# Performance work log

Measured on AMD Instinct MI355X. Metric: run time of the kernel, lower is better.

## Reference

```python
import jax, jax.numpy as jnp
import numpy as np

K = 2            # negative:positive edge ratio (init arg k)
N_NODES = 4096
N_EDGES = 8192
FEAT = 64


def setup_inputs() -> dict:
    key = jax.random.key(0)
    k1, k2, k3 = jax.random.split(key, 3)
    node_feature = jax.random.normal(k1, (N_NODES, FEAT), dtype=jnp.float32)
    edge_src = jax.random.randint(k2, (N_EDGES,), 0, N_NODES, dtype=jnp.int32)
    edge_dst = jax.random.randint(k3, (N_EDGES,), 0, N_NODES, dtype=jnp.int32)
    return {"node_feature": node_feature, "edge_src": edge_src, "edge_dst": edge_dst}


def reference(node_feature, edge_src, edge_dst):
    E = edge_src.shape[0]
    N = node_feature.shape[0]
    # [E, E] pairwise mask: candidate column j is valid for row i iff
    # dst[j] != dst[i] and dst[j] != src[i]
    valid = (edge_dst[:, None] != edge_dst[None, :]) & (edge_src[:, None] != edge_dst[None, :])
    # unsorted_segment_min over rows grouped by edge_src -> [N, E]
    segmin = jax.ops.segment_min(valid.astype(jnp.int8), edge_src, num_segments=N)
    # gather back per edge -> [E, E], flatten
    m = segmin[edge_src].reshape(-1).astype(bool)  # [E*E]
    num_negatives = jnp.sum(m)
    ratio = num_negatives // E                      # integer ratio as in TF code
    keep_prob = (K / ratio).astype(jnp.float32)
    u = jax.random.uniform(jax.random.key(42), (E * E,), dtype=jnp.float32)
    keep = m & (u < keep_prob)
    # fixed-size (jit-friendly) stand-in for tf.boolean_mask: expected count is K*E;
    # pad/truncate to exactly K*E kept flat indices (fill_value=0 pads).
    idx = jnp.nonzero(keep, size=K * E, fill_value=0)[0]
    rows = idx // E
    cols = idx % E
    edge_src_neg = edge_src[rows]
    edge_dst_neg = edge_dst[cols]
    return edge_src_neg, edge_dst_neg
```

## Files before the change

kernel.cpp:

```cpp
#include <hip/hip_runtime.h>
#include <stdint.h>
#include <math.h>

typedef unsigned int u32;
typedef unsigned long long u64;

#define E_CNT   8192
#define N_CNT   4096
#define TOT_N   (1u << 26)
#define OUT_K   16384
#define NODE_BM_WORDS 128
#define N_CHUNKS 1024

#define OFF_BAD      0x000000
#define OFF_CNT_DST  0x200000
#define OFF_CNT_SRC  0x204000
#define OFF_CCOUNT   0x208000
#define OFF_SCALARS  0x209000
#define OFF_KEEPBM   0x210000
#define ZERO_BYTES   0x209040

__device__ __forceinline__ u32 rotl32(u32 x, u32 d) {
  return __builtin_amdgcn_alignbit(x, x, 32u - d);
}

__device__ __forceinline__ void threefry4_0_42(u32 ia, u32 ib, u32 ic, u32 id,
                                               u32& ra, u32& rb, u32& rc, u32& rd) {
  const u32 k1 = 42u, k2 = 0x1BD11BF0u;
  u32 A0 = 0u, A1 = ia + k1;
  u32 B0 = 0u, B1 = ib + k1;
  u32 C0 = 0u, C1 = ic + k1;
  u32 D0 = 0u, D1 = id + k1;
#define R4(r) { A0 += A1; B0 += B1; C0 += C1; D0 += D1; \
  A1 = rotl32(A1, r); B1 = rotl32(B1, r); C1 = rotl32(C1, r); D1 = rotl32(D1, r); \
  A1 ^= A0; B1 ^= B0; C1 ^= C0; D1 ^= D0; }
#define INJ(c0, c1) { A0 += (c0); B0 += (c0); C0 += (c0); D0 += (c0); \
  A1 += (c1); B1 += (c1); C1 += (c1); D1 += (c1); }
#define INJ1(c1) { A1 += (c1); B1 += (c1); C1 += (c1); D1 += (c1); }
  R4(13) R4(15) R4(26) R4(6)
  INJ(k1, k2 + 1u)
  R4(17) R4(29) R4(16) R4(24)
  INJ(k2, 2u)
  R4(13) R4(15) R4(26) R4(6)
  INJ1(k1 + 3u)
  R4(17) R4(29) R4(16) R4(24)
  INJ(k1, k2 + 4u)
  R4(13) R4(15) R4(26) R4(6)
  INJ(k2, 5u)
#undef R4
#undef INJ
#undef INJ1
  ra = A0 ^ A1;
  rb = B0 ^ B1;
  rc = C0 ^ C1;
  rd = D0 ^ D1;
}

__global__ void k_build(const int* __restrict__ src, const int* __restrict__ dst,
                        u32* __restrict__ bad, u32* __restrict__ cnt_dst,
                        u32* __restrict__ cnt_src, int* __restrict__ out) {
  int tid = blockIdx.x * 256 + threadIdx.x;
  if (tid < N_CNT) {
    atomicOr(&bad[(u32)tid * NODE_BM_WORDS + ((u32)tid >> 5)], 1u << (tid & 31));
  }
  u32 s = (u32)src[tid], d = (u32)dst[tid];
  atomicOr(&bad[s * NODE_BM_WORDS + (d >> 5)], 1u << (d & 31));
  atomicAdd(&cnt_dst[d], 1u);
  atomicAdd(&cnt_src[s], 1u);
  int s0 = src[0], d0 = dst[0];
  out[tid] = s0;            out[tid + E_CNT] = s0;
  out[OUT_K + tid] = d0;    out[OUT_K + tid + E_CNT] = d0;
}

__global__ void __launch_bounds__(1024) k_rowcount(const u32* __restrict__ bad,
                                                   const u32* __restrict__ cnt_dst,
                                                   const u32* __restrict__ cnt_src,
                                                   u32* __restrict__ scal) {
  int wv = threadIdx.x >> 6, ln = threadIdx.x & 63;
  int n = blockIdx.x * 16 + wv;
  const u32* row = bad + (u32)n * NODE_BM_WORDS;
  u32 sum = 0;
#pragma unroll
  for (int h = 0; h < 2; ++h) {
    int w = ln + h * 64;
    u32 bits = row[w];
    while (bits) { int b = __ffs(bits) - 1; sum += cnt_dst[(w << 5) + b]; bits &= bits - 1; }
  }
#pragma unroll
  for (int off = 32; off > 0; off >>= 1) sum += __shfl_down(sum, off, 64);
  __shared__ u32 part[16];
  if (ln == 0) part[wv] = ((u32)E_CNT - sum) * cnt_src[n];
  __syncthreads();
  if (threadIdx.x == 0) {
    u32 tot = 0;
#pragma unroll
    for (int k = 0; k < 16; ++k) tot += part[k];
    atomicAdd(&scal[0], tot);
    __threadfence();
    if (atomicAdd(&scal[1], 1u) == 255u) {
      u32 nn = atomicAdd(&scal[0], 0u);
      u32 ratio = nn >> 13;
      float kp = 2.0f / (float)ratio;
      u32 T = (u32)ceil((double)kp * 8388608.0);
      u32 T9 = (T >= (1u << 23)) ? 0xFFFFFFFFu : (T << 9);
      atomicExch(&scal[2], T9);
    }
  }
}

__global__ void __launch_bounds__(1024) k_sample(const int* __restrict__ src,
                                                 const int* __restrict__ dst,
                                                 const u32* __restrict__ bad,
                                                 const u32* __restrict__ scal,
                                                 u64* __restrict__ keep_bm,
                                                 u32* __restrict__ ccount) {
  u32 wv = threadIdx.x >> 6, ln = threadIdx.x & 63;
  u32 i0w = blockIdx.x * 8192u + wv * 512u;
  u32 T9 = scal[2];
  u64 words[8];
  u64 any = 0;
#pragma unroll
  for (int h = 0; h < 2; ++h) {
    u32 i0 = i0w + (u32)h * 256u + ln;
    u32 b0, b1, b2, b3;
    threefry4_0_42(i0, i0 + 64u, i0 + 128u, i0 + 192u, b0, b1, b2, b3);
    u64 m0 = __ballot(b0 < T9);
    u64 m1 = __ballot(b1 < T9);
    u64 m2 = __ballot(b2 < T9);
    u64 m3 = __ballot(b3 < T9);
    words[4 * h]     = m0;
    words[4 * h + 1] = m1;
    words[4 * h + 2] = m2;
    words[4 * h + 3] = m3;
    any |= m0 | m1 | m2 | m3;
  }
  if (any) {
#pragma unroll
    for (int k = 0; k < 8; ++k) {
      if (words[k]) {
        u32 i = i0w + (u32)k * 64u + ln;
        bool kp = (words[k] >> ln) & 1ull;
        if (kp) {
          u32 n = (u32)src[i >> 13]; u32 v = (u32)dst[i & 8191];
          kp = ((bad[n * NODE_BM_WORDS + (v >> 5)] >> (v & 31)) & 1u) == 0u;
        }
        words[k] = __ballot(kp);
      }
    }
  }
  if (ln == 0) {
    u32 widx = i0w >> 6;
    ulonglong2* p = (ulonglong2*)&keep_bm[widx];
    p[0] = make_ulonglong2(words[0], words[1]);
    p[1] = make_ulonglong2(words[2], words[3]);
    p[2] = make_ulonglong2(words[4], words[5]);
    p[3] = make_ulonglong2(words[6], words[7]);
    u32 c = 0;
#pragma unroll
    for (int k = 0; k < 8; ++k) c += (u32)__popcll(words[k]);
    if (c) atomicAdd(&ccount[i0w >> 16], c);
  }
}

__global__ void k_compact(const int* __restrict__ src, const int* __restrict__ dst,
                          const u64* __restrict__ keep_bm, const u32* __restrict__ ccount,
                          int* __restrict__ out) {
  int c = blockIdx.x;
  int t = threadIdx.x;
  int wvid = t >> 6, ln = t & 63;
  __shared__ u32 red[4];
  __shared__ u32 wsum[4];

  u32 part = 0;
#pragma unroll
  for (int k = 0; k < 4; ++k) {
    int q = t + k * 256;
    u32 vq = ccount[q];
    part += (q < c) ? vq : 0u;
  }
  u32 r = part;
#pragma unroll
  for (int off = 32; off > 0; off >>= 1) r += __shfl_down(r, off, 64);
  if (ln == 0) red[wvid] = r;

  const u64* words = keep_bm + (size_t)c * 1024;
  u64 w[4];
  u32 cnt = 0;
#pragma unroll
  for (int k = 0; k < 4; ++k) { w[k] = words[4 * t + k]; cnt += (u32)__popcll(w[k]); }

  u32 scan = cnt;
#pragma unroll
  for (int off = 1; off < 64; off <<= 1) {
    u32 x = __shfl_up(scan, off, 64);
    if (ln >= off) scan += x;
  }
  if (ln == 63) wsum[wvid] = scan;
  __syncthreads();
  u32 coff_c = red[0] + red[1] + red[2] + red[3];
  u32 wbase = 0;
#pragma unroll
  for (int k = 0; k < 4; ++k) wbase += (k < wvid) ? wsum[k] : 0u;

  u32 rank = coff_c + wbase + scan - cnt;
  u32 tbase = (u32)c * 65536u + (u32)t * 256u;
#pragma unroll
  for (int k = 0; k < 4; ++k) {
    u64 bits = w[k];
    while (bits) {
      int b = __ffsll((unsigned long long)bits) - 1;
      if (rank < OUT_K) {
        u32 tt = tbase + (u32)k * 64u + (u32)b;
        out[rank]         = src[tt >> 13];
        out[OUT_K + rank] = dst[tt & 8191];
      }
      rank++;
      bits &= bits - 1;
    }
  }
}

extern "C" void kernel_launch(void* const* d_in, const int* in_sizes, int n_in,
                              void* d_out, int out_size, void* d_ws, size_t ws_size,
                              hipStream_t stream) {
  const int* src = (const int*)d_in[1];
  const int* dst = (const int*)d_in[2];
  int* out = (int*)d_out;
  char* ws = (char*)d_ws;

  u32* bad     = (u32*)(ws + OFF_BAD);
  u32* cnt_dst = (u32*)(ws + OFF_CNT_DST);
  u32* cnt_src = (u32*)(ws + OFF_CNT_SRC);
  u32* ccount  = (u32*)(ws + OFF_CCOUNT);
  u32* scal    = (u32*)(ws + OFF_SCALARS);
  u64* keep_bm = (u64*)(ws + OFF_KEEPBM);

  hipMemsetAsync(ws, 0, ZERO_BYTES, stream);
  k_build<<<E_CNT / 256, 256, 0, stream>>>(src, dst, bad, cnt_dst, cnt_src, out);
  k_rowcount<<<N_CNT / 16, 1024, 0, stream>>>(bad, cnt_dst, cnt_src, scal);
  k_sample<<<TOT_N / 8192, 1024, 0, stream>>>(src, dst, bad, scal, keep_bm, ccount);
  k_compact<<<N_CHUNKS, 256, 0, stream>>>(src, dst, keep_bm, ccount, out);
}
```

Measured before the change: 186.8 us.

## Fuse compaction into sampling kernel via decoupled look-back scan

Merges the sampling and compaction kernels into one. It uses a dynamic block ID and a decoupled look-back prefix scan over per-block descriptors, then scatters kept edges with mbcnt-based ranks. This removes the keep bitmap round-trip through memory and one kernel launch. The padding fill moves to the last block. In exchange, blocks now serialize on look-back spinning across 8192 blocks, and the memset grows to cover the descriptors.

Measured after the change: 223.2 us. 19.5% more time.

```diff
diff --git a/kernel.cpp b/kernel.cpp
--- a/kernel.cpp
+++ b/kernel.cpp
@@ -10,18 +10,22 @@
 #define TOT_N   (1u << 26)
 #define OUT_K   16384
 #define NODE_BM_WORDS 128
-#define N_CHUNKS 1024
+#define N_BLKS  8192
 
 #define OFF_BAD      0x000000
 #define OFF_CNT_DST  0x200000
 #define OFF_CNT_SRC  0x204000
-#define OFF_CCOUNT   0x208000
-#define OFF_SCALARS  0x209000
-#define OFF_KEEPBM   0x210000
-#define ZERO_BYTES   0x209040
+#define OFF_SCALARS  0x208000
+#define OFF_DESC     0x210000
+#define ZERO_BYTES   0x220000
 
 __device__ __forceinline__ u32 rotl32(u32 x, u32 d) {
   return __builtin_amdgcn_alignbit(x, x, 32u - d);
+}
+
+__device__ __forceinline__ u32 mbcnt64(u64 m) {
+  return __builtin_amdgcn_mbcnt_hi((u32)(m >> 32),
+         __builtin_amdgcn_mbcnt_lo((u32)m, 0u));
 }
 
 __device__ __forceinline__ void threefry4_0_42(u32 ia, u32 ib, u32 ic, u32 id,
@@ -58,7 +62,7 @@
 
 __global__ void k_build(const int* __restrict__ src, const int* __restrict__ dst,
                         u32* __restrict__ bad, u32* __restrict__ cnt_dst,
-                        u32* __restrict__ cnt_src, int* __restrict__ out) {
+                        u32* __restrict__ cnt_src) {
   int tid = blockIdx.x * 256 + threadIdx.x;
   if (tid < N_CNT) {
     atomicOr(&bad[(u32)tid * NODE_BM_WORDS + ((u32)tid >> 5)], 1u << (tid & 31));
@@ -67,9 +71,6 @@
   atomicOr(&bad[s * NODE_BM_WORDS + (d >> 5)], 1u << (d & 31));
   atomicAdd(&cnt_dst[d], 1u);
   atomicAdd(&cnt_src[s], 1u);
-  int s0 = src[0], d0 = dst[0];
-  out[tid] = s0;            out[tid + E_CNT] = s0;
-  out[OUT_K + tid] = d0;    out[OUT_K + tid + E_CNT] = d0;
 }
 
 __global__ void __launch_bounds__(1024) k_rowcount(const u32* __restrict__ bad,
@@ -111,12 +112,21 @@
 __global__ void __launch_bounds__(1024) k_sample(const int* __restrict__ src,
                                                  const int* __restrict__ dst,
                                                  const u32* __restrict__ bad,
-                                                 const u32* __restrict__ scal,
-                                                 u64* __restrict__ keep_bm,
-                                                 u32* __restrict__ ccount) {
-  u32 wv = threadIdx.x >> 6, ln = threadIdx.x & 63;
-  u32 i0w = blockIdx.x * 8192u + wv * 512u;
-  u32 T9 = scal[2];
+                                                 u32* __restrict__ scal,
+                                                 u64* __restrict__ desc,
+                                                 int* __restrict__ out) {
+  __shared__ u32 sh_cnt[16];
+  __shared__ u32 sh_vb;
+  __shared__ u32 sh_excl;
+  const u32 t = threadIdx.x;
+  const u32 wv = t >> 6, ln = t & 63;
+
+  if (t == 0) sh_vb = atomicAdd(&scal[3], 1u);
+  __syncthreads();
+  const u32 vb = sh_vb;
+  const u32 T9 = scal[2];
+  const u32 i0w = vb * 8192u + wv * 512u;
+
   u64 words[8];
   u64 any = 0;
 #pragma unroll
@@ -148,74 +158,71 @@
       }
     }
   }
-  if (ln == 0) {
-    u32 widx = i0w >> 6;
-    ulonglong2* p = (ulonglong2*)&keep_bm[widx];
-    p[0] = make_ulonglong2(words[0], words[1]);
-    p[1] = make_ulonglong2(words[2], words[3]);
-    p[2] = make_ulonglong2(words[4], words[5]);
-    p[3] = make_ulonglong2(words[6], words[7]);
-    u32 c = 0;
-#pragma unroll
-    for (int k = 0; k < 8; ++k) c += (u32)__popcll(words[k]);
-    if (c) atomicAdd(&ccount[i0w >> 16], c);
-  }
-}
-
-__global__ void k_compact(const int* __restrict__ src, const int* __restrict__ dst,
-                          const u64* __restrict__ keep_bm, const u32* __restrict__ ccount,
-                          int* __restrict__ out) {
-  int c = blockIdx.x;
-  int t = threadIdx.x;
-  int wvid = t >> 6, ln = t & 63;
-  __shared__ u32 red[4];
-  __shared__ u32 wsum[4];
-
-  u32 part = 0;
-#pragma unroll
-  for (int k = 0; k < 4; ++k) {
-    int q = t + k * 256;
-    u32 vq = ccount[q];
-    part += (q < c) ? vq : 0u;
-  }
-  u32 r = part;
-#pragma unroll
-  for (int off = 32; off > 0; off >>= 1) r += __shfl_down(r, off, 64);
-  if (ln == 0) red[wvid] = r;
-
-  const u64* words = keep_bm + (size_t)c * 1024;
-  u64 w[4];
-  u32 cnt = 0;
-#pragma unroll
-  for (int k = 0; k < 4; ++k) { w[k] = words[4 * t + k]; cnt += (u32)__popcll(w[k]); }
-
-  u32 scan = cnt;
-#pragma unroll
-  for (int off = 1; off < 64; off <<= 1) {
-    u32 x = __shfl_up(scan, off, 64);
-    if (ln >= off) scan += x;
-  }
-  if (ln == 63) wsum[wvid] = scan;
-  __syncthreads();
-  u32 coff_c = red[0] + red[1] + red[2] + red[3];
-  u32 wbase = 0;
-#pragma unroll
-  for (int k = 0; k < 4; ++k) wbase += (k < wvid) ? wsum[k] : 0u;
-
-  u32 rank = coff_c + wbase + scan - cnt;
-  u32 tbase = (u32)c * 65536u + (u32)t * 256u;
-#pragma unroll
-  for (int k = 0; k < 4; ++k) {
-    u64 bits = w[k];
-    while (bits) {
-      int b = __ffsll((unsigned long long)bits) - 1;
+  u32 wcnt = 0;
+#pragma unroll
+  for (int k = 0; k < 8; ++k) wcnt += (u32)__popcll(words[k]);
+  if (ln == 0) sh_cnt[wv] = wcnt;
+  __syncthreads();
+
+  if (wv == 0) {
+    u32 tot = 0;
+#pragma unroll
+    for (int k = 0; k < 16; ++k) tot += sh_cnt[k];
+    if (ln == 0) atomicExch(&desc[vb], (1ull << 32) | (u64)tot);
+    u32 excl = 0;
+    if (vb != 0u) {
+      int base = (int)vb - 1;
+      for (;;) {
+        int idx = base - (int)ln;
+        u64 d = (idx >= 0) ? atomicAdd(&desc[idx], 0ull) : (2ull << 32);
+        u32 flag = (u32)(d >> 32);
+        u64 incl_m = __ballot(flag == 2u);
+        u64 nr_m   = __ballot(flag == 0u);
+        int fi = incl_m ? (__ffsll((unsigned long long)incl_m) - 1) : 64;
+        int fn = nr_m   ? (__ffsll((unsigned long long)nr_m)   - 1) : 64;
+        if (fn < fi) { __builtin_amdgcn_s_sleep(1); continue; }
+        u32 contrib = ((int)ln <= fi) ? (u32)d : 0u;
+#pragma unroll
+        for (int off = 32; off > 0; off >>= 1) contrib += __shfl_down(contrib, off, 64);
+        excl += __shfl(contrib, 0, 64);
+        if (fi < 64) break;
+        base -= 64;
+        if (base < 0) break;
+      }
+    }
+    if (ln == 0) {
+      atomicExch(&desc[vb], (2ull << 32) | (u64)(excl + tot));
+      sh_excl = excl;
+    }
+  }
+  __syncthreads();
+
+  u32 wexcl = sh_excl;
+#pragma unroll
+  for (int k = 0; k < 16; ++k) wexcl += ((u32)k < wv) ? sh_cnt[k] : 0u;
+  u32 rbase = wexcl;
+#pragma unroll
+  for (int k = 0; k < 8; ++k) {
+    u64 wk = words[k];
+    if ((wk >> ln) & 1ull) {
+      u32 rank = rbase + mbcnt64(wk);
       if (rank < OUT_K) {
-        u32 tt = tbase + (u32)k * 64u + (u32)b;
-        out[rank]         = src[tt >> 13];
-        out[OUT_K + rank] = dst[tt & 8191];
+        u32 i = i0w + (u32)k * 64u + ln;
+        out[rank]         = src[i >> 13];
+        out[OUT_K + rank] = dst[i & 8191];
       }
-      rank++;
-      bits &= bits - 1;
+    }
+    rbase += (u32)__popcll(wk);
+  }
+
+  if (vb == (u32)(N_BLKS - 1)) {
+    u32 tot = 0;
+#pragma unroll
+    for (int k = 0; k < 16; ++k) tot += sh_cnt[k];
+    u32 total = sh_excl + tot;
+    int s0 = src[0], d0 = dst[0];
+    for (u32 p = total + t; p < OUT_K; p += 1024u) {
+      out[p] = s0; out[OUT_K + p] = d0;
     }
   }
 }
@@ -231,13 +238,11 @@
   u32* bad     = (u32*)(ws + OFF_BAD);
   u32* cnt_dst = (u32*)(ws + OFF_CNT_DST);
   u32* cnt_src = (u32*)(ws + OFF_CNT_SRC);
-  u32* ccount  = (u32*)(ws + OFF_CCOUNT);
   u32* scal    = (u32*)(ws + OFF_SCALARS);
-  u64* keep_bm = (u64*)(ws + OFF_KEEPBM);
+  u64* desc    = (u64*)(ws + OFF_DESC);
 
   hipMemsetAsync(ws, 0, ZERO_BYTES, stream);
-  k_build<<<E_CNT / 256, 256, 0, stream>>>(src, dst, bad, cnt_dst, cnt_src, out);
+  k_build<<<E_CNT / 256, 256, 0, stream>>>(src, dst, bad, cnt_dst, cnt_src);
   k_rowcount<<<N_CNT / 16, 1024, 0, stream>>>(bad, cnt_dst, cnt_src, scal);
-  k_sample<<<TOT_N / 8192, 1024, 0, stream>>>(src, dst, bad, scal, keep_bm, ccount);
-  k_compact<<<N_CHUNKS, 256, 0, stream>>>(src, dst, keep_bm, ccount, out);
-}
+  k_sample<<<N_BLKS, 1024, 0, stream>>>(src, dst, bad, scal, desc, out);
+}
```

## Fuse build, rowcount and sample kernels into one persistent-style kernel with atomic tickets

Applied to the files above, without the earlier changes.

Merges the bitmap build and row-count passes into the sampling kernel. Blocks take a ticket from an atomic counter and coordinate through spin-waits on global flags, which removes two kernel launches and their inter-kernel gaps. The cost is that every sampling block busy-waits until the threshold is published. Correctness depends on the first-ticketed blocks being resident, and reads of bad, cnt_dst and cnt_src now go through atomics.

Result: slower. 218.9 us (+17.2%).

```diff
diff --git a/kernel.cpp b/kernel.cpp
--- a/kernel.cpp
+++ b/kernel.cpp
@@ -18,11 +18,19 @@
 #define OFF_CCOUNT   0x208000
 #define OFF_SCALARS  0x209000
 #define OFF_KEEPBM   0x210000
-#define ZERO_BYTES   0x209040
+#define ZERO_BYTES   0x209140
+
+#define SC_TICKET  0
+#define SC_BDONE   16
+#define SC_NUMNEG  32
+#define SC_RCDONE  33
+#define SC_T9      64
 
 __device__ __forceinline__ u32 rotl32(u32 x, u32 d) {
   return __builtin_amdgcn_alignbit(x, x, 32u - d);
 }
+
+__device__ __forceinline__ u32 aread(u32* p) { return atomicAdd(p, 0u); }
 
 __device__ __forceinline__ void threefry4_0_42(u32 ia, u32 ib, u32 ic, u32 id,
                                                u32& ra, u32& rb, u32& rc, u32& rd) {
@@ -56,67 +64,83 @@
   rd = D0 ^ D1;
 }
 
-__global__ void k_build(const int* __restrict__ src, const int* __restrict__ dst,
-                        u32* __restrict__ bad, u32* __restrict__ cnt_dst,
-                        u32* __restrict__ cnt_src, int* __restrict__ out) {
-  int tid = blockIdx.x * 256 + threadIdx.x;
-  if (tid < N_CNT) {
-    atomicOr(&bad[(u32)tid * NODE_BM_WORDS + ((u32)tid >> 5)], 1u << (tid & 31));
-  }
-  u32 s = (u32)src[tid], d = (u32)dst[tid];
-  atomicOr(&bad[s * NODE_BM_WORDS + (d >> 5)], 1u << (d & 31));
-  atomicAdd(&cnt_dst[d], 1u);
-  atomicAdd(&cnt_src[s], 1u);
-  int s0 = src[0], d0 = dst[0];
-  out[tid] = s0;            out[tid + E_CNT] = s0;
-  out[OUT_K + tid] = d0;    out[OUT_K + tid + E_CNT] = d0;
-}
-
-__global__ void __launch_bounds__(1024) k_rowcount(const u32* __restrict__ bad,
-                                                   const u32* __restrict__ cnt_dst,
-                                                   const u32* __restrict__ cnt_src,
-                                                   u32* __restrict__ scal) {
-  int wv = threadIdx.x >> 6, ln = threadIdx.x & 63;
-  int n = blockIdx.x * 16 + wv;
-  const u32* row = bad + (u32)n * NODE_BM_WORDS;
-  u32 sum = 0;
-#pragma unroll
-  for (int h = 0; h < 2; ++h) {
-    int w = ln + h * 64;
-    u32 bits = row[w];
-    while (bits) { int b = __ffs(bits) - 1; sum += cnt_dst[(w << 5) + b]; bits &= bits - 1; }
-  }
-#pragma unroll
-  for (int off = 32; off > 0; off >>= 1) sum += __shfl_down(sum, off, 64);
-  __shared__ u32 part[16];
-  if (ln == 0) part[wv] = ((u32)E_CNT - sum) * cnt_src[n];
-  __syncthreads();
-  if (threadIdx.x == 0) {
-    u32 tot = 0;
-#pragma unroll
-    for (int k = 0; k < 16; ++k) tot += part[k];
-    atomicAdd(&scal[0], tot);
-    __threadfence();
-    if (atomicAdd(&scal[1], 1u) == 255u) {
-      u32 nn = atomicAdd(&scal[0], 0u);
-      u32 ratio = nn >> 13;
-      float kp = 2.0f / (float)ratio;
-      u32 T = (u32)ceil((double)kp * 8388608.0);
-      u32 T9 = (T >= (1u << 23)) ? 0xFFFFFFFFu : (T << 9);
-      atomicExch(&scal[2], T9);
-    }
-  }
-}
-
 __global__ void __launch_bounds__(1024) k_sample(const int* __restrict__ src,
                                                  const int* __restrict__ dst,
-                                                 const u32* __restrict__ bad,
-                                                 const u32* __restrict__ scal,
+                                                 u32* __restrict__ bad,
+                                                 u32* __restrict__ cnt_dst,
+                                                 u32* __restrict__ cnt_src,
+                                                 u32* __restrict__ scal,
+                                                 u32* __restrict__ ccount,
                                                  u64* __restrict__ keep_bm,
-                                                 u32* __restrict__ ccount) {
-  u32 wv = threadIdx.x >> 6, ln = threadIdx.x & 63;
-  u32 i0w = blockIdx.x * 8192u + wv * 512u;
-  u32 T9 = scal[2];
+                                                 int* __restrict__ out) {
+  const u32 t = threadIdx.x;
+  const u32 wv = t >> 6, ln = t & 63;
+  __shared__ u32 sh_vb, sh_t9;
+  __shared__ u32 part[16];
+
+  if (t == 0) sh_vb = atomicAdd(&scal[SC_TICKET], 1u);
+  __syncthreads();
+  const u32 vb = sh_vb;
+
+  if (vb < 8u) {
+    u32 e = vb * 1024u + t;
+    if (e < N_CNT) {
+      atomicOr(&bad[e * NODE_BM_WORDS + (e >> 5)], 1u << (e & 31));
+    }
+    u32 s = (u32)src[e], d = (u32)dst[e];
+    atomicOr(&bad[s * NODE_BM_WORDS + (d >> 5)], 1u << (d & 31));
+    atomicAdd(&cnt_dst[d], 1u);
+    atomicAdd(&cnt_src[s], 1u);
+    int s0 = src[0], d0 = dst[0];
+    out[e] = s0;            out[e + E_CNT] = s0;
+    out[OUT_K + e] = d0;    out[OUT_K + e + E_CNT] = d0;
+    __threadfence();
+    __syncthreads();
+    if (t == 0) atomicAdd(&scal[SC_BDONE], 1u);
+  }
+
+  if (vb < 256u) {
+    if (t == 0) { while (aread(&scal[SC_BDONE]) < 8u) __builtin_amdgcn_s_sleep(2); }
+    __syncthreads();
+    u32 n = vb * 16u + wv;
+    u32 rb = n * NODE_BM_WORDS;
+    u32 sum = 0;
+#pragma unroll
+    for (int h = 0; h < 2; ++h) {
+      u32 w = ln + (u32)h * 64u;
+      u32 bits = aread(&bad[rb + w]);
+      while (bits) { int b = __ffs(bits) - 1; sum += aread(&cnt_dst[(w << 5) + b]); bits &= bits - 1; }
+    }
+#pragma unroll
+    for (int off = 32; off > 0; off >>= 1) sum += __shfl_down(sum, off, 64);
+    if (ln == 0) part[wv] = ((u32)E_CNT - sum) * aread(&cnt_src[n]);
+    __syncthreads();
+    if (t == 0) {
+      u32 tot = 0;
+#pragma unroll
+      for (int k = 0; k < 16; ++k) tot += part[k];
+      atomicAdd(&scal[SC_NUMNEG], tot);
+      __threadfence();
+      if (atomicAdd(&scal[SC_RCDONE], 1u) == 255u) {
+        u32 nn = aread(&scal[SC_NUMNEG]);
+        u32 ratio = nn >> 13;
+        float kp = 2.0f / (float)ratio;
+        u32 T = (u32)ceil((double)kp * 8388608.0);
+        u32 T9 = (T >= (1u << 23)) ? 0xFFFFFFFFu : (T << 9);
+        atomicExch(&scal[SC_T9], T9);
+      }
+    }
+  }
+
+  if (t == 0) {
+    u32 v;
+    while ((v = aread(&scal[SC_T9])) == 0u) __builtin_amdgcn_s_sleep(8);
+    sh_t9 = v;
+  }
+  __syncthreads();
+  const u32 T9 = sh_t9;
+
+  const u32 i0w = blockIdx.x * 8192u + wv * 512u;
   u64 words[8];
   u64 any = 0;
 #pragma unroll
@@ -142,7 +166,7 @@
         bool kp = (words[k] >> ln) & 1ull;
         if (kp) {
           u32 n = (u32)src[i >> 13]; u32 v = (u32)dst[i & 8191];
-          kp = ((bad[n * NODE_BM_WORDS + (v >> 5)] >> (v & 31)) & 1u) == 0u;
+          kp = ((aread(&bad[n * NODE_BM_WORDS + (v >> 5)]) >> (v & 31)) & 1u) == 0u;
         }
         words[k] = __ballot(kp);
       }
@@ -236,8 +260,7 @@
   u64* keep_bm = (u64*)(ws + OFF_KEEPBM);
 
   hipMemsetAsync(ws, 0, ZERO_BYTES, stream);
-  k_build<<<E_CNT / 256, 256, 0, stream>>>(src, dst, bad, cnt_dst, cnt_src, out);
-  k_rowcount<<<N_CNT / 16, 1024, 0, stream>>>(bad, cnt_dst, cnt_src, scal);
-  k_sample<<<TOT_N / 8192, 1024, 0, stream>>>(src, dst, bad, scal, keep_bm, ccount);
+  k_sample<<<TOT_N / 8192, 1024, 0, stream>>>(src, dst, bad, cnt_dst, cnt_src,
+                                              scal, ccount, keep_bm, out);
   k_compact<<<N_CHUNKS, 256, 0, stream>>>(src, dst, keep_bm, ccount, out);
 }
```
